# Performance work log

Measured on AMD Instinct MI355X. Metric: run time of the kernel, lower is better.

The kernel has to match this reference:

```python
import jax, jax.numpy as jnp
import numpy as np

N, E = 50000, 800000
IN_C, HID, HEADS, LAT = 128, 64, 2, 32
NEG_SLOPE = 0.2  # PyG GATConv default LeakyReLU slope


def gat_layer(x, src, dst, W, att_src, att_dst, bias, heads, out_ch, concat, n):
    # Linear projection, per-head: [n, heads, out_ch]
    h = (x @ W).reshape(n, heads, out_ch)
    a_src = jnp.einsum('nhc,hc->nh', h, att_src)  # [n, heads]
    a_dst = jnp.einsum('nhc,hc->nh', h, att_dst)
    # Per-edge attention logits (edge j->i uses src j, dst i)
    alpha = jax.nn.leaky_relu(a_src[src] + a_dst[dst], negative_slope=NEG_SLOPE)  # [e, heads]
    # Segment softmax over incoming edges of each destination node
    amax = jax.ops.segment_max(alpha, dst, num_segments=n)
    ealpha = jnp.exp(alpha - amax[dst])
    denom = jax.ops.segment_sum(ealpha, dst, num_segments=n)
    alpha = ealpha / (denom[dst] + 1e-16)
    # Weighted scatter-aggregate of source features
    msg = h[src] * alpha[:, :, None]  # [e, heads, out_ch]
    out = jax.ops.segment_sum(msg, dst, num_segments=n)  # [n, heads, out_ch]
    out = out.reshape(n, heads * out_ch) if concat else out.mean(axis=1)
    return out + bias


def setup_inputs() -> dict:
    key = jax.random.key(0)
    ks = jax.random.split(key, 16)
    x = jax.random.normal(ks[0], (N, IN_C), dtype=jnp.float32)
    edge_index = jax.random.randint(ks[1], (2, E), 0, N, dtype=jnp.int32).astype(jnp.int64)
    s = 0.1
    W1 = jax.random.normal(ks[2], (IN_C, HEADS * HID), dtype=jnp.float32) * s
    att_src1 = jax.random.normal(ks[3], (HEADS, HID), dtype=jnp.float32) * s
    att_dst1 = jax.random.normal(ks[4], (HEADS, HID), dtype=jnp.float32) * s
    b1 = jnp.zeros((HEADS * HID,), dtype=jnp.float32)
    Wmu = jax.random.normal(ks[5], (HEADS * HID, LAT), dtype=jnp.float32) * s
    att_src_mu = jax.random.normal(ks[6], (1, LAT), dtype=jnp.float32) * s
    att_dst_mu = jax.random.normal(ks[7], (1, LAT), dtype=jnp.float32) * s
    bmu = jnp.zeros((LAT,), dtype=jnp.float32)
    Wlv = jax.random.normal(ks[8], (HEADS * HID, LAT), dtype=jnp.float32) * s
    att_src_lv = jax.random.normal(ks[9], (1, LAT), dtype=jnp.float32) * s
    att_dst_lv = jax.random.normal(ks[10], (1, LAT), dtype=jnp.float32) * s
    blv = jnp.zeros((LAT,), dtype=jnp.float32)
    return {"x": x, "edge_index": edge_index, "W1": W1, "att_src1": att_src1,
            "att_dst1": att_dst1, "b1": b1, "Wmu": Wmu, "att_src_mu": att_src_mu,
            "att_dst_mu": att_dst_mu, "bmu": bmu, "Wlv": Wlv,
            "att_src_lv": att_src_lv, "att_dst_lv": att_dst_lv, "blv": blv}


def reference(x, edge_index, W1, att_src1, att_dst1, b1,
              Wmu, att_src_mu, att_dst_mu, bmu,
              Wlv, att_src_lv, att_dst_lv, blv):
    n = x.shape[0]
    # PyG GATConv adds self-loops by default
    loops = jnp.arange(n, dtype=edge_index.dtype)
    src = jnp.concatenate([edge_index[0], loops])
    dst = jnp.concatenate([edge_index[1], loops])
    h = gat_layer(x, src, dst, W1, att_src1, att_dst1, b1, HEADS, HID, True, n)
    h = jax.nn.elu(h)
    mu = gat_layer(h, src, dst, Wmu, att_src_mu, att_dst_mu, bmu, 1, LAT, False, n)
    logvar = gat_layer(h, src, dst, Wlv, att_src_lv, att_dst_lv, blv, 1, LAT, False, n)
    return (mu, logvar)
```

## Files before the change

kernel.cpp:

```cpp
#include <hip/hip_runtime.h>
#include <hip/hip_bf16.h>

#define N_NODES 50000
#define N_EDGES 800000
#define EP (N_EDGES + N_NODES)
#define IN_C 128
#define HID 64
#define HEADS 2
#define LAT 32
#define NEG_SLOPE 0.2f
#define MAXDEG 256
#define NBUCKET 391
#define BCAP 3072
#define CHUNK 2048
#define NSCAT ((EP + CHUNK - 1) / CHUNK)
#define NPROJ1 ((N_NODES + 31) / 32)

typedef __attribute__((ext_vector_type(8))) short bf16x8;
typedef __attribute__((ext_vector_type(4))) float f32x4;

__device__ __forceinline__ unsigned short f2bf(float f) {
  unsigned u = __float_as_uint(f);
  u += 0x7FFF + ((u >> 16) & 1);
  return (unsigned short)(u >> 16);
}
__device__ __forceinline__ float bf_lo(unsigned u) { return __uint_as_float(u << 16); }
__device__ __forceinline__ float bf_hi(unsigned u) { return __uint_as_float(u & 0xFFFF0000u); }

__device__ __forceinline__ bf16x8 pack_bf8(const float* __restrict__ p) {
  float4 a = *(const float4*)p;
  float4 b = *(const float4*)(p + 4);
  bf16x8 r;
  r[0] = (short)f2bf(a.x); r[1] = (short)f2bf(a.y);
  r[2] = (short)f2bf(a.z); r[3] = (short)f2bf(a.w);
  r[4] = (short)f2bf(b.x); r[5] = (short)f2bf(b.y);
  r[6] = (short)f2bf(b.z); r[7] = (short)f2bf(b.w);
  return r;
}

__global__ __launch_bounds__(256) void prep_kernel(
    const float* __restrict__ W1, const float* __restrict__ Wmu,
    const float* __restrict__ Wlv, int* __restrict__ cursor,
    unsigned short* __restrict__ Wb1g, unsigned short* __restrict__ Wb2g) {
  const int b = blockIdx.x, t = threadIdx.x;
  if (b == 0) {
    for (int i = t; i < NBUCKET; i += 256) cursor[i] = 0;
  } else if (b <= 64) {
    int i = (b - 1) * 256 + t;
    int k = i >> 7, n = i & 127;
    int kk = k >> 5, q = (k >> 3) & 3, j = k & 7;
    Wb1g[((((kk << 2) + q) << 7) + n) * 8 + j] = f2bf(W1[i]);
  } else {
    int i = (b - 65) * 256 + t;
    int k = i >> 6, n = i & 63;
    float v = (n < 32) ? Wmu[k * 32 + n] : Wlv[k * 32 + (n - 32)];
    int kk = k >> 5, q = (k >> 3) & 3, j = k & 7;
    Wb2g[((((kk << 2) + q) << 6) + n) * 8 + j] = f2bf(v);
  }
}

struct ScatSmem {
  int histL[512];
  int baseL[512];
  int gbaseL[512];
  int wsumS[4];
  int nvalS;
  unsigned staging[CHUNK];
  unsigned short bktidL[CHUNK];
};
union K1Smem { ScatSmem sc; float part[32][4]; };

__global__ __launch_bounds__(256) void k1_kernel(
    const int* __restrict__ ei, int* __restrict__ cursor,
    unsigned* __restrict__ csr,
    const float* __restrict__ x, const unsigned short* __restrict__ Wb1g,
    const float* __restrict__ att_src, const float* __restrict__ att_dst,
    unsigned short* __restrict__ h1b, float* __restrict__ a1) {
  __shared__ K1Smem sm;
  const int t = threadIdx.x, lane = t & 63, wid = t >> 6;

  if (blockIdx.x < NSCAT) {
    for (int i = t; i < 512; i += 256) sm.sc.histL[i] = 0;
    __syncthreads();
    int myb[CHUNK / 256];
    int myloc[CHUNK / 256];
    unsigned mypay[CHUNK / 256];
    #pragma unroll
    for (int i = 0; i < CHUNK / 256; ++i) {
      int e = blockIdx.x * CHUNK + i * 256 + t;
      if (e < EP) {
        int s, d;
        if (e < N_EDGES) { s = ei[e]; d = ei[N_EDGES + e]; }
        else { s = d = e - N_EDGES; }
        int b = d >> 7;
        myb[i] = b;
        mypay[i] = ((unsigned)(d & 127) << 17) | (unsigned)s;
        myloc[i] = atomicAdd(&sm.sc.histL[b], 1);
      } else myb[i] = -1;
    }
    __syncthreads();
    {
      int v0 = sm.sc.histL[2 * t], v1 = sm.sc.histL[2 * t + 1];
      int pair = v0 + v1, inc = pair;
      #pragma unroll
      for (int off = 1; off < 64; off <<= 1) {
        int nv = __shfl_up(inc, off);
        if (lane >= off) inc += nv;
      }
      if (lane == 63) sm.sc.wsumS[wid] = inc;
      __syncthreads();
      if (t == 0) {
        int run = 0;
        #pragma unroll
        for (int w = 0; w < 4; ++w) { int c = sm.sc.wsumS[w]; sm.sc.wsumS[w] = run; run += c; }
        sm.sc.nvalS = run;
      }
      __syncthreads();
      int excl = sm.sc.wsumS[wid] + inc - pair;
      sm.sc.baseL[2 * t] = excl;
      sm.sc.baseL[2 * t + 1] = excl + v0;
    }
    __syncthreads();
    #pragma unroll
    for (int i = 0; i < CHUNK / 256; ++i)
      if (myb[i] >= 0) {
        int p = sm.sc.baseL[myb[i]] + myloc[i];
        sm.sc.staging[p] = mypay[i];
        sm.sc.bktidL[p] = (unsigned short)myb[i];
      }
    for (int b = t; b < NBUCKET; b += 256) {
      int c = sm.sc.histL[b];
      sm.sc.gbaseL[b] = c ? atomicAdd(&cursor[b], c) : 0;
    }
    __syncthreads();
    const int nval = sm.sc.nvalS;
    for (int j = t; j < nval; j += 256) {
      int b = sm.sc.bktidL[j];
      int off = sm.sc.gbaseL[b] + (j - sm.sc.baseL[b]);
      if (off < BCAP) csr[b * BCAP + off] = sm.sc.staging[j];
    }
  } else {
    const int pb = blockIdx.x - NSCAT;
    if (t < 128) ((float*)sm.part)[t] = 0.f;
    __syncthreads();
    const int w = wid;
    const int m = lane & 15, quad = lane >> 4;
    const int row0 = pb * 32;
    const int n0 = w * 32;
    const int head = w >> 1;
    f32x4 acc[2][2] = {};
    #pragma unroll
    for (int kk = 0; kk < 4; ++kk) {
      bf16x8 afr[2], bfr[2];
      #pragma unroll
      for (int mt = 0; mt < 2; ++mt) {
        int row = row0 + mt * 16 + m;
        if (row >= N_NODES) row = N_NODES - 1;
        afr[mt] = pack_bf8(x + (size_t)row * 128 + kk * 32 + quad * 8);
      }
      #pragma unroll
      for (int nt = 0; nt < 2; ++nt)
        bfr[nt] = *(const bf16x8*)&Wb1g[((((kk << 2) + quad) << 7) + n0 + nt * 16 + m) * 8];
      #pragma unroll
      for (int mt = 0; mt < 2; ++mt)
        #pragma unroll
        for (int nt = 0; nt < 2; ++nt)
          acc[mt][nt] = __builtin_amdgcn_mfma_f32_16x16x32_bf16(
              afr[mt], bfr[nt], acc[mt][nt], 0, 0, 0);
    }
    float asv[2], adv[2];
    #pragma unroll
    for (int nt = 0; nt < 2; ++nt) {
      int cc = ((n0 & 63) + nt * 16 + m);
      asv[nt] = att_src[head * HID + cc];
      adv[nt] = att_dst[head * HID + cc];
    }
    #pragma unroll
    for (int mt = 0; mt < 2; ++mt)
      #pragma unroll
      for (int r = 0; r < 4; ++r) {
        int row = row0 + mt * 16 + quad * 4 + r;
        if (row < N_NODES) {
          #pragma unroll
          for (int nt = 0; nt < 2; ++nt)
            h1b[(size_t)row * 128 + n0 + nt * 16 + m] = f2bf(acc[mt][nt][r]);
        }
        float s = acc[mt][0][r] * asv[0] + acc[mt][1][r] * asv[1];
        float d = acc[mt][0][r] * adv[0] + acc[mt][1][r] * adv[1];
        #pragma unroll
        for (int off = 8; off; off >>= 1) {
          s += __shfl_xor(s, off);
          d += __shfl_xor(d, off);
        }
        if (m == 0) {
          atomicAdd(&sm.part[mt * 16 + quad * 4 + r][head], s);
          atomicAdd(&sm.part[mt * 16 + quad * 4 + r][2 + head], d);
        }
      }
    __syncthreads();
    if (t < 32) {
      int row = row0 + t;
      if (row < N_NODES)
        *(float4*)&a1[(size_t)row * 4] = make_float4(
            sm.part[t][0], sm.part[t][1], sm.part[t][2], sm.part[t][3]);
    }
  }
}

__global__ __launch_bounds__(256) void bucket_fill_kernel(
    const int* __restrict__ cursor, unsigned* __restrict__ csr,
    int* __restrict__ counts, int* __restrict__ cend) {
  __shared__ unsigned eseg[BCAP];
  __shared__ int hist[128];
  __shared__ int basef[128];
  __shared__ int cur[128];
  const int b = blockIdx.x, t = threadIdx.x;
  const int segbase = b * BCAP;
  int cnt = cursor[b];
  if (cnt > BCAP) cnt = BCAP;
  if (t < 128) hist[t] = 0;
  __syncthreads();
  for (int j = t; j < cnt; j += 256) {
    unsigned u = csr[segbase + j];
    eseg[j] = u;
    atomicAdd(&hist[u >> 17], 1);
  }
  __syncthreads();
  if (t < 64) {
    int v0 = hist[2 * t], v1 = hist[2 * t + 1];
    int pair = v0 + v1, inc = pair;
    #pragma unroll
    for (int off = 1; off < 64; off <<= 1) {
      int nv = __shfl_up(inc, off);
      if (t >= off) inc += nv;
    }
    int excl = inc - pair;
    basef[2 * t] = excl;
    basef[2 * t + 1] = excl + v0;
  }
  __syncthreads();
  if (t < 128) {
    cur[t] = basef[t];
    int n = b * 128 + t;
    if (n < N_NODES) {
      counts[n] = hist[t];
      cend[n] = segbase + basef[t] + hist[t];
    }
  }
  __syncthreads();
  for (int j = t; j < cnt; j += 256) {
    unsigned u = eseg[j];
    int dl = u >> 17;
    int p = atomicAdd(&cur[dl], 1);
    csr[segbase + p] = u & 0x1FFFF;
  }
}

__global__ __launch_bounds__(256) void agg1_csr_kernel(
    const int* __restrict__ counts, const int* __restrict__ cend,
    const unsigned* __restrict__ csr_src, const float4* __restrict__ a1,
    const unsigned* __restrict__ h1b2, const float* __restrict__ b,
    float* __restrict__ hact) {
  __shared__ float2 w_lds[4][MAXDEG];
  __shared__ int   s_lds[4][MAXDEG];
  const int t = threadIdx.x, wid = t >> 6, lane = t & 63;
  const int n = blockIdx.x * 4 + wid;
  const int end = cend[n];
  int cnt = counts[n];
  if (cnt > MAXDEG) cnt = MAXDEG;
  const int beg = end - cnt;
  const float4 bv = a1[n];
  float p0 = 0.f, p1 = 0.f;
  for (int i = lane; i < cnt; i += 64) {
    int s = (int)csr_src[beg + i];
    float4 av = a1[s];
    float l0 = av.x + bv.z; l0 = l0 > 0.f ? l0 : NEG_SLOPE * l0;
    float l1 = av.y + bv.w; l1 = l1 > 0.f ? l1 : NEG_SLOPE * l1;
    float e0 = expf(l0), e1 = expf(l1);
    w_lds[wid][i] = make_float2(e0, e1);
    s_lds[wid][i] = s;
    p0 += e0; p1 += e1;
  }
  #pragma unroll
  for (int off = 32; off; off >>= 1) {
    p0 += __shfl_xor(p0, off);
    p1 += __shfl_xor(p1, off);
  }
  __syncthreads();
  const int g = lane >> 4;
  const int lq = lane & 15;
  const int head = lq >> 3;
  float acc[8] = {0.f, 0.f, 0.f, 0.f, 0.f, 0.f, 0.f, 0.f};
  #pragma unroll 2
  for (int i = g; i < cnt; i += 4) {
    int s = s_lds[wid][i];
    float w = ((const float*)&w_lds[wid][i])[head];
    uint4 u = *(const uint4*)(h1b2 + (size_t)s * 64 + lq * 4);
    acc[0] += bf_lo(u.x) * w; acc[1] += bf_hi(u.x) * w;
    acc[2] += bf_lo(u.y) * w; acc[3] += bf_hi(u.y) * w;
    acc[4] += bf_lo(u.z) * w; acc[5] += bf_hi(u.z) * w;
    acc[6] += bf_lo(u.w) * w; acc[7] += bf_hi(u.w) * w;
  }
  #pragma unroll
  for (int j = 0; j < 8; ++j) {
    acc[j] += __shfl_xor(acc[j], 16);
    acc[j] += __shfl_xor(acc[j], 32);
  }
  if (g == 0) {
    float inv = 1.f / ((head ? p1 : p0) + 1e-16f);
    float o[8];
    #pragma unroll
    for (int j = 0; j < 8; ++j) {
      float v = acc[j] * inv + b[lq * 8 + j];
      o[j] = v > 0.f ? v : (expf(v) - 1.f);
    }
    float4* dst = (float4*)(hact + (size_t)n * 128 + lq * 8);
    dst[0] = make_float4(o[0], o[1], o[2], o[3]);
    dst[1] = make_float4(o[4], o[5], o[6], o[7]);
  }
}

__global__ __launch_bounds__(256) void proj2_kernel(
    const float* __restrict__ h, const unsigned short* __restrict__ Wb2g,
    const float* __restrict__ asmu, const float* __restrict__ admu,
    const float* __restrict__ aslv, const float* __restrict__ adlv,
    unsigned short* __restrict__ h2b, float* __restrict__ a2) {
  const int t = threadIdx.x;
  const int w = t >> 6, lane = t & 63;
  const int m = lane & 15, quad = lane >> 4;
  const int row0 = blockIdx.x * 64 + (w >> 1) * 32;
  const int j = w & 1;
  const int n0 = j * 32;
  f32x4 acc[2][2] = {};
  #pragma unroll
  for (int kk = 0; kk < 4; ++kk) {
    bf16x8 afr[2], bfr[2];
    #pragma unroll
    for (int mt = 0; mt < 2; ++mt) {
      int row = row0 + mt * 16 + m;
      if (row >= N_NODES) row = N_NODES - 1;
      afr[mt] = pack_bf8(h + (size_t)row * 128 + kk * 32 + quad * 8);
    }
    #pragma unroll
    for (int nt = 0; nt < 2; ++nt)
      bfr[nt] = *(const bf16x8*)&Wb2g[((((kk << 2) + quad) << 6) + n0 + nt * 16 + m) * 8];
    #pragma unroll
    for (int mt = 0; mt < 2; ++mt)
      #pragma unroll
      for (int nt = 0; nt < 2; ++nt)
        acc[mt][nt] = __builtin_amdgcn_mfma_f32_16x16x32_bf16(
            afr[mt], bfr[nt], acc[mt][nt], 0, 0, 0);
  }
  float asv[2], adv[2];
  #pragma unroll
  for (int nt = 0; nt < 2; ++nt) {
    int o = nt * 16 + m;
    asv[nt] = (j ? aslv : asmu)[o];
    adv[nt] = (j ? adlv : admu)[o];
  }
  #pragma unroll
  for (int mt = 0; mt < 2; ++mt)
    #pragma unroll
    for (int r = 0; r < 4; ++r) {
      int row = row0 + mt * 16 + quad * 4 + r;
      if (row < N_NODES) {
        #pragma unroll
        for (int nt = 0; nt < 2; ++nt)
          h2b[(size_t)row * 64 + n0 + nt * 16 + m] = f2bf(acc[mt][nt][r]);
      }
      float s = acc[mt][0][r] * asv[0] + acc[mt][1][r] * asv[1];
      float d = acc[mt][0][r] * adv[0] + acc[mt][1][r] * adv[1];
      #pragma unroll
      for (int off = 8; off; off >>= 1) {
        s += __shfl_xor(s, off);
        d += __shfl_xor(d, off);
      }
      if (m == 0 && row < N_NODES) {
        a2[(size_t)row * 4 + j * 2 + 0] = s;
        a2[(size_t)row * 4 + j * 2 + 1] = d;
      }
    }
}

__global__ __launch_bounds__(256) void agg2_csr_kernel(
    const int* __restrict__ counts, const int* __restrict__ cend,
    const unsigned* __restrict__ csr_src, const float4* __restrict__ a2,
    const unsigned* __restrict__ h2b2,
    const float* __restrict__ bmu, const float* __restrict__ blv,
    float* __restrict__ out) {
  __shared__ float2 w_lds[4][MAXDEG];
  __shared__ int   s_lds[4][MAXDEG];
  const int t = threadIdx.x, wid = t >> 6, lane = t & 63;
  const int n = blockIdx.x * 4 + wid;
  const int end = cend[n];
  int cnt = counts[n];
  if (cnt > MAXDEG) cnt = MAXDEG;
  const int beg = end - cnt;
  const float4 bv = a2[n];
  float p0 = 0.f, p1 = 0.f;
  for (int i = lane; i < cnt; i += 64) {
    int s = (int)csr_src[beg + i];
    float4 av = a2[s];
    float l0 = av.x + bv.y; l0 = l0 > 0.f ? l0 : NEG_SLOPE * l0;
    float l1 = av.z + bv.w; l1 = l1 > 0.f ? l1 : NEG_SLOPE * l1;
    float e0 = expf(l0), e1 = expf(l1);
    w_lds[wid][i] = make_float2(e0, e1);
    s_lds[wid][i] = s;
    p0 += e0; p1 += e1;
  }
  #pragma unroll
  for (int off = 32; off; off >>= 1) {
    p0 += __shfl_xor(p0, off);
    p1 += __shfl_xor(p1, off);
  }
  __syncthreads();
  const int g = lane >> 3;
  const int lq = lane & 7;
  const int j = lq >> 2;
  float acc[8] = {0.f, 0.f, 0.f, 0.f, 0.f, 0.f, 0.f, 0.f};
  #pragma unroll 2
  for (int i = g; i < cnt; i += 8) {
    int s = s_lds[wid][i];
    float w = ((const float*)&w_lds[wid][i])[j];
    uint4 u = *(const uint4*)(h2b2 + (size_t)s * 32 + lq * 4);
    acc[0] += bf_lo(u.x) * w; acc[1] += bf_hi(u.x) * w;
    acc[2] += bf_lo(u.y) * w; acc[3] += bf_hi(u.y) * w;
    acc[4] += bf_lo(u.z) * w; acc[5] += bf_hi(u.z) * w;
    acc[6] += bf_lo(u.w) * w; acc[7] += bf_hi(u.w) * w;
  }
  #pragma unroll
  for (int jj = 0; jj < 8; ++jj) {
    acc[jj] += __shfl_xor(acc[jj], 8);
    acc[jj] += __shfl_xor(acc[jj], 16);
    acc[jj] += __shfl_xor(acc[jj], 32);
  }
  if (g == 0) {
    float inv = 1.f / ((j ? p1 : p0) + 1e-16f);
    const float* bb = j ? blv : bmu;
    const int o = (lq & 3) * 8;
    float r[8];
    #pragma unroll
    for (int jj = 0; jj < 8; ++jj) r[jj] = acc[jj] * inv + bb[o + jj];
    float4* dst = (float4*)(out + (size_t)j * N_NODES * LAT + (size_t)n * LAT + o);
    dst[0] = make_float4(r[0], r[1], r[2], r[3]);
    dst[1] = make_float4(r[4], r[5], r[6], r[7]);
  }
}

extern "C" void kernel_launch(void* const* d_in, const int* in_sizes, int n_in,
                              void* d_out, int out_size, void* d_ws, size_t ws_size,
                              hipStream_t stream) {
  const float* x        = (const float*)d_in[0];
  const int* ei         = (const int*)d_in[1];
  const float* W1       = (const float*)d_in[2];
  const float* att_src1 = (const float*)d_in[3];
  const float* att_dst1 = (const float*)d_in[4];
  const float* b1       = (const float*)d_in[5];
  const float* Wmu      = (const float*)d_in[6];
  const float* asmu     = (const float*)d_in[7];
  const float* admu     = (const float*)d_in[8];
  const float* bmu      = (const float*)d_in[9];
  const float* Wlv      = (const float*)d_in[10];
  const float* aslv     = (const float*)d_in[11];
  const float* adlv     = (const float*)d_in[12];
  const float* blv      = (const float*)d_in[13];
  float* out = (float*)d_out;

  float* ws   = (float*)d_ws;
  float* hact = ws;
  float* a1   = hact + (size_t)N_NODES * 128;
  float* a2   = a1 + (size_t)N_NODES * 4;
  unsigned short* h1b = (unsigned short*)(a2 + (size_t)N_NODES * 4);
  unsigned short* h2b = h1b + (size_t)N_NODES * 128;
  unsigned short* Wb1g = h2b + (size_t)N_NODES * 64;
  unsigned short* Wb2g = Wb1g + 16384;
  int* counts = (int*)(Wb2g + 8192);
  int* cend   = counts + N_NODES;
  int* cursor = cend + N_NODES;
  unsigned* csr = (unsigned*)(cursor + NBUCKET);

  prep_kernel<<<97, 256, 0, stream>>>(W1, Wmu, Wlv, cursor, Wb1g, Wb2g);

  k1_kernel<<<NSCAT + NPROJ1, 256, 0, stream>>>(
      ei, cursor, csr, x, Wb1g, att_src1, att_dst1, h1b, a1);
  bucket_fill_kernel<<<NBUCKET, 256, 0, stream>>>(cursor, csr, counts, cend);
  agg1_csr_kernel<<<N_NODES / 4, 256, 0, stream>>>(
      counts, cend, csr, (const float4*)a1, (const unsigned*)h1b, b1, hact);
  proj2_kernel<<<(N_NODES + 63) / 64, 256, 0, stream>>>(
      hact, Wb2g, asmu, admu, aslv, adlv, h2b, a2);
  agg2_csr_kernel<<<N_NODES / 4, 256, 0, stream>>>(
      counts, cend, csr, (const float4*)a2, (const unsigned*)h2b, bmu, blv, out);
}
```

Measured before the change: 217.3 us.

## Fuse layer-1 aggregation with layer-2 projection via shared-memory rows

```diff
diff --git a/kernel.cpp b/kernel.cpp
--- a/kernel.cpp
+++ b/kernel.cpp
@@ -10,6 +10,7 @@
 #define LAT 32
 #define NEG_SLOPE 0.2f
 #define MAXDEG 256
+#define MAXDEG1 128
 #define NBUCKET 391
 #define BCAP 3072
 #define CHUNK 2048
@@ -256,130 +257,118 @@
   }
 }
 
-__global__ __launch_bounds__(256) void agg1_csr_kernel(
+__global__ __launch_bounds__(256) void agg1_proj2_kernel(
     const int* __restrict__ counts, const int* __restrict__ cend,
     const unsigned* __restrict__ csr_src, const float4* __restrict__ a1,
     const unsigned* __restrict__ h1b2, const float* __restrict__ b,
-    float* __restrict__ hact) {
-  __shared__ float2 w_lds[4][MAXDEG];
-  __shared__ int   s_lds[4][MAXDEG];
-  const int t = threadIdx.x, wid = t >> 6, lane = t & 63;
-  const int n = blockIdx.x * 4 + wid;
-  const int end = cend[n];
-  int cnt = counts[n];
-  if (cnt > MAXDEG) cnt = MAXDEG;
-  const int beg = end - cnt;
-  const float4 bv = a1[n];
-  float p0 = 0.f, p1 = 0.f;
-  for (int i = lane; i < cnt; i += 64) {
-    int s = (int)csr_src[beg + i];
-    float4 av = a1[s];
-    float l0 = av.x + bv.z; l0 = l0 > 0.f ? l0 : NEG_SLOPE * l0;
-    float l1 = av.y + bv.w; l1 = l1 > 0.f ? l1 : NEG_SLOPE * l1;
-    float e0 = expf(l0), e1 = expf(l1);
-    w_lds[wid][i] = make_float2(e0, e1);
-    s_lds[wid][i] = s;
-    p0 += e0; p1 += e1;
-  }
-  #pragma unroll
-  for (int off = 32; off; off >>= 1) {
-    p0 += __shfl_xor(p0, off);
-    p1 += __shfl_xor(p1, off);
-  }
-  __syncthreads();
-  const int g = lane >> 4;
-  const int lq = lane & 15;
-  const int head = lq >> 3;
-  float acc[8] = {0.f, 0.f, 0.f, 0.f, 0.f, 0.f, 0.f, 0.f};
-  #pragma unroll 2
-  for (int i = g; i < cnt; i += 4) {
-    int s = s_lds[wid][i];
-    float w = ((const float*)&w_lds[wid][i])[head];
-    uint4 u = *(const uint4*)(h1b2 + (size_t)s * 64 + lq * 4);
-    acc[0] += bf_lo(u.x) * w; acc[1] += bf_hi(u.x) * w;
-    acc[2] += bf_lo(u.y) * w; acc[3] += bf_hi(u.y) * w;
-    acc[4] += bf_lo(u.z) * w; acc[5] += bf_hi(u.z) * w;
-    acc[6] += bf_lo(u.w) * w; acc[7] += bf_hi(u.w) * w;
-  }
-  #pragma unroll
-  for (int j = 0; j < 8; ++j) {
-    acc[j] += __shfl_xor(acc[j], 16);
-    acc[j] += __shfl_xor(acc[j], 32);
-  }
-  if (g == 0) {
-    float inv = 1.f / ((head ? p1 : p0) + 1e-16f);
-    float o[8];
-    #pragma unroll
-    for (int j = 0; j < 8; ++j) {
-      float v = acc[j] * inv + b[lq * 8 + j];
-      o[j] = v > 0.f ? v : (expf(v) - 1.f);
-    }
-    float4* dst = (float4*)(hact + (size_t)n * 128 + lq * 8);
-    dst[0] = make_float4(o[0], o[1], o[2], o[3]);
-    dst[1] = make_float4(o[4], o[5], o[6], o[7]);
-  }
-}
-
-__global__ __launch_bounds__(256) void proj2_kernel(
-    const float* __restrict__ h, const unsigned short* __restrict__ Wb2g,
+    const unsigned short* __restrict__ Wb2g,
     const float* __restrict__ asmu, const float* __restrict__ admu,
     const float* __restrict__ aslv, const float* __restrict__ adlv,
     unsigned short* __restrict__ h2b, float* __restrict__ a2) {
-  const int t = threadIdx.x;
-  const int w = t >> 6, lane = t & 63;
+  __shared__ __align__(16) float2 w_lds[16][MAXDEG1];
+  __shared__ __align__(16) int    s_lds[16][MAXDEG1];
+  __shared__ __align__(16) float  sm_a2[16][4];
+  const int t = threadIdx.x, wid = t >> 6, lane = t & 63;
+  if (t < 64) ((float*)sm_a2)[t] = 0.f;
+  const int nbase = blockIdx.x * 16;
+
+  int cnt_r[4];
+  float p0r[4], p1r[4];
+  #pragma unroll
+  for (int nd = 0; nd < 4; ++nd) {
+    const int slot = wid * 4 + nd;
+    const int n = nbase + slot;
+    const int end = cend[n];
+    int cnt = counts[n]; if (cnt > MAXDEG1) cnt = MAXDEG1;
+    const int beg = end - cnt;
+    cnt_r[nd] = cnt;
+    const float4 bv = a1[n];
+    float p0 = 0.f, p1 = 0.f;
+    for (int i = lane; i < cnt; i += 64) {
+      int s = (int)csr_src[beg + i];
+      float4 av = a1[s];
+      float l0 = av.x + bv.z; l0 = l0 > 0.f ? l0 : NEG_SLOPE * l0;
+      float l1 = av.y + bv.w; l1 = l1 > 0.f ? l1 : NEG_SLOPE * l1;
+      float e0 = expf(l0), e1 = expf(l1);
+      w_lds[slot][i] = make_float2(e0, e1);
+      s_lds[slot][i] = s;
+      p0 += e0; p1 += e1;
+    }
+    #pragma unroll
+    for (int off = 32; off; off >>= 1) {
+      p0 += __shfl_xor(p0, off);
+      p1 += __shfl_xor(p1, off);
+    }
+    p0r[nd] = p0; p1r[nd] = p1;
+  }
+
+  const int g = lane >> 4, lq = lane & 15, head = lq >> 3;
+  #pragma unroll
+  for (int nd = 0; nd < 4; ++nd) {
+    const int slot = wid * 4 + nd;
+    const int cnt = cnt_r[nd];
+    float acc[8] = {0.f, 0.f, 0.f, 0.f, 0.f, 0.f, 0.f, 0.f};
+    #pragma unroll 2
+    for (int i = g; i < cnt; i += 4) {
+      int s = s_lds[slot][i];
+      float w = ((const float*)&w_lds[slot][i])[head];
+      uint4 u = *(const uint4*)(h1b2 + (size_t)s * 64 + lq * 4);
+      acc[0] += bf_lo(u.x) * w; acc[1] += bf_hi(u.x) * w;
+      acc[2] += bf_lo(u.y) * w; acc[3] += bf_hi(u.y) * w;
+      acc[4] += bf_lo(u.z) * w; acc[5] += bf_hi(u.z) * w;
+      acc[6] += bf_lo(u.w) * w; acc[7] += bf_hi(u.w) * w;
+    }
+    #pragma unroll
+    for (int jj = 0; jj < 8; ++jj) {
+      acc[jj] += __shfl_xor(acc[jj], 16);
+      acc[jj] += __shfl_xor(acc[jj], 32);
+    }
+    if (g == 0) {
+      float inv = 1.f / ((head ? p1r[nd] : p0r[nd]) + 1e-16f);
+      float o[8];
+      #pragma unroll
+      for (int jj = 0; jj < 8; ++jj) {
+        float v = acc[jj] * inv + b[lq * 8 + jj];
+        o[jj] = v > 0.f ? v : (expf(v) - 1.f);
+      }
+      float4* hrow = (float4*)s_lds[slot];
+      hrow[lq * 2 + 0] = make_float4(o[0], o[1], o[2], o[3]);
+      hrow[lq * 2 + 1] = make_float4(o[4], o[5], o[6], o[7]);
+    }
+  }
+  __syncthreads();
+
   const int m = lane & 15, quad = lane >> 4;
-  const int row0 = blockIdx.x * 64 + (w >> 1) * 32;
-  const int j = w & 1;
-  const int n0 = j * 32;
-  f32x4 acc[2][2] = {};
+  const int c = wid * 16 + m;
+  const int j = wid >> 1;
+  f32x4 acc2 = {};
   #pragma unroll
   for (int kk = 0; kk < 4; ++kk) {
-    bf16x8 afr[2], bfr[2];
-    #pragma unroll
-    for (int mt = 0; mt < 2; ++mt) {
-      int row = row0 + mt * 16 + m;
-      if (row >= N_NODES) row = N_NODES - 1;
-      afr[mt] = pack_bf8(h + (size_t)row * 128 + kk * 32 + quad * 8);
-    }
-    #pragma unroll
-    for (int nt = 0; nt < 2; ++nt)
-      bfr[nt] = *(const bf16x8*)&Wb2g[((((kk << 2) + quad) << 6) + n0 + nt * 16 + m) * 8];
-    #pragma unroll
-    for (int mt = 0; mt < 2; ++mt)
-      #pragma unroll
-      for (int nt = 0; nt < 2; ++nt)
-        acc[mt][nt] = __builtin_amdgcn_mfma_f32_16x16x32_bf16(
-            afr[mt], bfr[nt], acc[mt][nt], 0, 0, 0);
-  }
-  float asv[2], adv[2];
-  #pragma unroll
-  for (int nt = 0; nt < 2; ++nt) {
-    int o = nt * 16 + m;
-    asv[nt] = (j ? aslv : asmu)[o];
-    adv[nt] = (j ? adlv : admu)[o];
-  }
-  #pragma unroll
-  for (int mt = 0; mt < 2; ++mt)
-    #pragma unroll
-    for (int r = 0; r < 4; ++r) {
-      int row = row0 + mt * 16 + quad * 4 + r;
-      if (row < N_NODES) {
-        #pragma unroll
-        for (int nt = 0; nt < 2; ++nt)
-          h2b[(size_t)row * 64 + n0 + nt * 16 + m] = f2bf(acc[mt][nt][r]);
-      }
-      float s = acc[mt][0][r] * asv[0] + acc[mt][1][r] * asv[1];
-      float d = acc[mt][0][r] * adv[0] + acc[mt][1][r] * adv[1];
-      #pragma unroll
-      for (int off = 8; off; off >>= 1) {
-        s += __shfl_xor(s, off);
-        d += __shfl_xor(d, off);
-      }
-      if (m == 0 && row < N_NODES) {
-        a2[(size_t)row * 4 + j * 2 + 0] = s;
-        a2[(size_t)row * 4 + j * 2 + 1] = d;
-      }
-    }
+    bf16x8 af = pack_bf8((const float*)s_lds[m] + kk * 32 + quad * 8);
+    bf16x8 bf = *(const bf16x8*)&Wb2g[((((kk << 2) + quad) << 6) + c) * 8];
+    acc2 = __builtin_amdgcn_mfma_f32_16x16x32_bf16(af, bf, acc2, 0, 0, 0);
+  }
+  const float asv = (j ? aslv : asmu)[(wid & 1) * 16 + m];
+  const float adv = (j ? adlv : admu)[(wid & 1) * 16 + m];
+  #pragma unroll
+  for (int r = 0; r < 4; ++r) {
+    const int slot = quad * 4 + r;
+    h2b[(size_t)(nbase + slot) * 64 + c] = f2bf(acc2[r]);
+    float s = acc2[r] * asv, d = acc2[r] * adv;
+    #pragma unroll
+    for (int off = 8; off; off >>= 1) {
+      s += __shfl_xor(s, off);
+      d += __shfl_xor(d, off);
+    }
+    if (m == 0) {
+      atomicAdd(&sm_a2[slot][j * 2 + 0], s);
+      atomicAdd(&sm_a2[slot][j * 2 + 1], d);
+    }
+  }
+  __syncthreads();
+  if (t < 16)
+    *(float4*)&a2[(size_t)(nbase + t) * 4] = make_float4(
+        sm_a2[t][0], sm_a2[t][1], sm_a2[t][2], sm_a2[t][3]);
 }
 
 __global__ __launch_bounds__(256) void agg2_csr_kernel(
@@ -484,10 +473,9 @@
   k1_kernel<<<NSCAT + NPROJ1, 256, 0, stream>>>(
       ei, cursor, csr, x, Wb1g, att_src1, att_dst1, h1b, a1);
   bucket_fill_kernel<<<NBUCKET, 256, 0, stream>>>(cursor, csr, counts, cend);
-  agg1_csr_kernel<<<N_NODES / 4, 256, 0, stream>>>(
-      counts, cend, csr, (const float4*)a1, (const unsigned*)h1b, b1, hact);
-  proj2_kernel<<<(N_NODES + 63) / 64, 256, 0, stream>>>(
-      hact, Wb2g, asmu, admu, aslv, adlv, h2b, a2);
+  agg1_proj2_kernel<<<N_NODES / 16, 256, 0, stream>>>(
+      counts, cend, csr, (const float4*)a1, (const unsigned*)h1b, b1,
+      Wb2g, asmu, admu, aslv, adlv, h2b, a2);
   agg2_csr_kernel<<<N_NODES / 4, 256, 0, stream>>>(
       counts, cend, csr, (const float4*)a2, (const unsigned*)h2b, bmu, blv, out);
 }
```

New measurement: 216.9 us. No clear change (-0.2%).
